# Performance work log

Measured on AMD Instinct MI355X. Metric: run time of the kernel, lower is better.

## Reference

```python
import jax, jax.numpy as jnp
import numpy as np

B, C, H, W = 16, 512, 32, 32
EPS = 1e-5

def setup_inputs() -> dict:
    key = jax.random.key(0)
    ks = jax.random.split(key, 7)
    s = 1.0 / np.sqrt(C)
    return {
        "x": jax.random.normal(ks[0], (B, C, H, W), dtype=jnp.float32),
        "norm_w": jnp.ones((C,), jnp.float32),
        "norm_b": jnp.zeros((C,), jnp.float32),
        "qkv_w": jax.random.normal(ks[1], (3 * C, C), dtype=jnp.float32) * s,
        "qkv_b": jax.random.normal(ks[2], (3 * C,), dtype=jnp.float32) * 0.01,
        "out_w": jax.random.normal(ks[3], (C, C), dtype=jnp.float32) * s,
        "out_b": jax.random.normal(ks[4], (C,), dtype=jnp.float32) * 0.01,
    }

def reference(x, norm_w, norm_b, qkv_w, qkv_b, out_w, out_b):
    b, c, h, w = x.shape
    # GroupNorm with num_groups=1: normalize over (C,H,W) per sample, per-channel affine
    mean = jnp.mean(x, axis=(1, 2, 3), keepdims=True)
    var = jnp.var(x, axis=(1, 2, 3), keepdims=True)
    xn = (x - mean) * jax.lax.rsqrt(var + EPS)
    xn = xn * norm_w[None, :, None, None] + norm_b[None, :, None, None]
    # 1x1 conv QKV: [b,3c,h,w]
    qkv = jnp.einsum('bchw,oc->bohw', xn, qkv_w) + qkv_b[None, :, None, None]
    q, k, v = jnp.split(qkv, 3, axis=1)
    n = h * w
    q = q.transpose(0, 2, 3, 1).reshape(b, n, c)   # [b, N, c]
    k = k.reshape(b, c, n)                          # [b, c, N]
    v = v.transpose(0, 2, 3, 1).reshape(b, n, c)   # [b, N, c]
    scores = jnp.einsum('bnc,bcm->bnm', q, k) * (c ** -0.5)  # [b, N, N]
    attn = jax.nn.softmax(scores, axis=-1)
    out = jnp.einsum('bnm,bmc->bnc', attn, v)       # [b, N, c]
    out = out.reshape(b, h, w, c).transpose(0, 3, 1, 2)
    out = jnp.einsum('bchw,oc->bohw', out, out_w) + out_b[None, :, None, None]
    return out + x
```

## Files before the change

### kernel.cpp

```cpp
#include <hip/hip_runtime.h>
#include <math.h>

#define BATCH 16
#define CH    512
#define NTOK  1024
#define CHW   (CH * NTOK)
#define EPSV  1e-5f

typedef __attribute__((ext_vector_type(8))) short bf16x8;
typedef __attribute__((ext_vector_type(4))) float f32x4;

__device__ __forceinline__ unsigned short f2bf(float f) {
    union { float f; unsigned u; } cv; cv.f = f;
    unsigned r = cv.u + 0x7FFFu + ((cv.u >> 16) & 1u);
    return (unsigned short)(r >> 16);
}

static const size_t OFF_WQKV = 256;
static const size_t OFF_OW   = OFF_WQKV + 1572864;
static const size_t OFF_XNT  = OFF_OW   + 524288;
static const size_t OFF_QT   = OFF_XNT  + 16777216;
static const size_t OFF_KT   = OFF_QT   + 16777216;
static const size_t OFF_V    = OFF_KT   + 16777216;
static const size_t OFF_OT   = OFF_V    + 16777216;
static const size_t OFF_S    = OFF_OT   + 16777216;
static const size_t OFF_P    = OFF_S    + 67108864;

__global__ void k_zero_stats(float* ws) {
    if (threadIdx.x < 64) ws[threadIdx.x] = 0.0f;
}

__global__ __launch_bounds__(256) void k_stats_partial(const float* __restrict__ x, float* __restrict__ ws) {
    int blk   = blockIdx.x;
    int b     = blk >> 6;
    int chunk = blk & 63;
    const float4* xp = (const float4*)(x + (size_t)b * CHW + (size_t)chunk * 8192);
    int t = threadIdx.x;
    float s = 0.0f, ss = 0.0f;
#pragma unroll
    for (int j = 0; j < 8; j++) {
        float4 v = xp[t + j * 256];
        s  += v.x + v.y + v.z + v.w;
        ss += v.x * v.x + v.y * v.y + v.z * v.z + v.w * v.w;
    }
#pragma unroll
    for (int off = 32; off; off >>= 1) {
        s  += __shfl_xor(s, off, 64);
        ss += __shfl_xor(ss, off, 64);
    }
    __shared__ float ls[4], lss[4];
    int wave = t >> 6, lane = t & 63;
    if (lane == 0) { ls[wave] = s; lss[wave] = ss; }
    __syncthreads();
    if (t == 0) {
        atomicAdd(&ws[b], ls[0] + ls[1] + ls[2] + ls[3]);
        atomicAdd(&ws[16 + b], lss[0] + lss[1] + lss[2] + lss[3]);
    }
}

__global__ void k_stats_final(float* ws) {
    int b = threadIdx.x;
    if (b < 16) {
        float inv  = 1.0f / (float)CHW;
        float mean = ws[b] * inv;
        float var  = ws[16 + b] * inv - mean * mean;
        ws[32 + b] = mean;
        ws[48 + b] = rsqrtf(var + EPSV);
    }
}

__global__ __launch_bounds__(256) void k_cvt(const float* __restrict__ in, unsigned short* __restrict__ out, int n4) {
    int i = blockIdx.x * 256 + threadIdx.x;
    if (i < n4) {
        float4 v = ((const float4*)in)[i];
        ushort4 o;
        o.x = f2bf(v.x); o.y = f2bf(v.y); o.z = f2bf(v.z); o.w = f2bf(v.w);
        ((ushort4*)out)[i] = o;
    }
}

__global__ __launch_bounds__(256) void k_xnt(const float* __restrict__ x,
                                             const float* __restrict__ nw,
                                             const float* __restrict__ nb,
                                             const float* __restrict__ ws,
                                             unsigned short* __restrict__ xnt) {
    __shared__ float ls[64][65];
    int b  = blockIdx.z;
    int c0 = blockIdx.y * 64;
    int n0 = blockIdx.x * 64;
    float mean = ws[32 + b], rstd = ws[48 + b];
    int t = threadIdx.x;
    int cl = t >> 4, n4 = t & 15;
    const float* xb = x + (size_t)b * CHW;
#pragma unroll
    for (int i = 0; i < 4; i++) {
        int c = c0 + cl + i * 16;
        float a  = rstd * nw[c];
        float bb = nb[c] - mean * a;
        float4 v = *(const float4*)(xb + (size_t)c * NTOK + n0 + n4 * 4);
        ls[cl + i * 16][n4 * 4 + 0] = v.x * a + bb;
        ls[cl + i * 16][n4 * 4 + 1] = v.y * a + bb;
        ls[cl + i * 16][n4 * 4 + 2] = v.z * a + bb;
        ls[cl + i * 16][n4 * 4 + 3] = v.w * a + bb;
    }
    __syncthreads();
    int nl = t >> 4, c4 = t & 15;
    unsigned short* dst = xnt + (size_t)b * NTOK * CH;
#pragma unroll
    for (int i = 0; i < 4; i++) {
        int n = n0 + nl + i * 16;
        ushort4 o;
        o.x = f2bf(ls[c4 * 4 + 0][nl + i * 16]);
        o.y = f2bf(ls[c4 * 4 + 1][nl + i * 16]);
        o.z = f2bf(ls[c4 * 4 + 2][nl + i * 16]);
        o.w = f2bf(ls[c4 * 4 + 3][nl + i * 16]);
        *(ushort4*)(dst + (size_t)n * CH + c0 + c4 * 4) = o;
    }
}

__device__ __forceinline__ void mfma_core(const unsigned short* __restrict__ A, int lda,
                                          const unsigned short* __restrict__ B, int ldb,
                                          int K, int m0, int n0,
                                          unsigned short* sA, unsigned short* sB,
                                          f32x4 acc[4][4]) {
    const int t = threadIdx.x;
    const int w = t >> 6, lane = t & 63;
    const int wm = (w & 1) * 64, wn = (w >> 1) * 64;
    const int r16 = lane & 15, quad = lane >> 4;
#pragma unroll
    for (int i = 0; i < 4; i++)
#pragma unroll
        for (int j = 0; j < 4; j++) acc[i][j] = (f32x4){0.f, 0.f, 0.f, 0.f};
    const int row0 = t >> 2, kc0 = (t & 3) * 8;
    for (int k0 = 0; k0 < K; k0 += 32) {
        *(uint4*)(sA + (row0)      * 32 + kc0) = *(const uint4*)(A + (size_t)(m0 + row0)      * lda + k0 + kc0);
        *(uint4*)(sA + (row0 + 64) * 32 + kc0) = *(const uint4*)(A + (size_t)(m0 + row0 + 64) * lda + k0 + kc0);
        *(uint4*)(sB + (row0)      * 32 + kc0) = *(const uint4*)(B + (size_t)(n0 + row0)      * ldb + k0 + kc0);
        *(uint4*)(sB + (row0 + 64) * 32 + kc0) = *(const uint4*)(B + (size_t)(n0 + row0 + 64) * ldb + k0 + kc0);
        __syncthreads();
        bf16x8 af[4], bfr[4];
#pragma unroll
        for (int i = 0; i < 4; i++) af[i]  = *(const bf16x8*)(sA + (wm + i * 16 + r16) * 32 + quad * 8);
#pragma unroll
        for (int j = 0; j < 4; j++) bfr[j] = *(const bf16x8*)(sB + (wn + j * 16 + r16) * 32 + quad * 8);
#pragma unroll
        for (int i = 0; i < 4; i++)
#pragma unroll
            for (int j = 0; j < 4; j++)
                acc[i][j] = __builtin_amdgcn_mfma_f32_16x16x32_bf16(af[i], bfr[j], acc[i][j], 0, 0, 0);
        __syncthreads();
    }
}

__global__ __launch_bounds__(256) void k_gemm_qkv(const unsigned short* __restrict__ Wq,
                                                  const float* __restrict__ qb,
                                                  const unsigned short* __restrict__ XNT,
                                                  unsigned short* __restrict__ QT,
                                                  unsigned short* __restrict__ KT,
                                                  unsigned short* __restrict__ V) {
    __shared__ __align__(16) unsigned short sA[128 * 32];
    __shared__ __align__(16) unsigned short sB[128 * 32];
    const int b  = blockIdx.z;
    const int m0 = blockIdx.y * 128;
    const int n0 = blockIdx.x * 128;
    f32x4 acc[4][4];
    mfma_core(Wq, CH, XNT + (size_t)b * NTOK * CH, CH, CH, m0, n0, sA, sB, acc);
    const int t = threadIdx.x;
    const int w = t >> 6, lane = t & 63;
    const int wm = (w & 1) * 64, wn = (w >> 1) * 64;
    const int r16 = lane & 15, quad = lane >> 4;
    const int region = m0 >> 9;
    unsigned short* dstT = (region == 0) ? QT : KT;
#pragma unroll
    for (int i = 0; i < 4; i++) {
        const int o0g = m0 + wm + i * 16 + quad * 4;
        const int ro  = o0g & 511;
#pragma unroll
        for (int j = 0; j < 4; j++) {
            const int col = n0 + wn + j * 16 + r16;
            f32x4 a = acc[i][j];
            if (region < 2) {
                ushort4 pk;
                pk.x = f2bf(a[0] + qb[o0g + 0]);
                pk.y = f2bf(a[1] + qb[o0g + 1]);
                pk.z = f2bf(a[2] + qb[o0g + 2]);
                pk.w = f2bf(a[3] + qb[o0g + 3]);
                *(ushort4*)(dstT + (size_t)b * NTOK * CH + (size_t)col * CH + ro) = pk;
            } else {
#pragma unroll
                for (int r = 0; r < 4; r++)
                    V[(size_t)b * CH * NTOK + (size_t)(ro + r) * NTOK + col] = f2bf(a[r] + qb[o0g + r]);
            }
        }
    }
}

__global__ __launch_bounds__(256) void k_gemm_sc(const unsigned short* __restrict__ QT,
                                                 const unsigned short* __restrict__ KT,
                                                 float* __restrict__ S) {
    __shared__ __align__(16) unsigned short sA[128 * 32];
    __shared__ __align__(16) unsigned short sB[128 * 32];
    const int b  = blockIdx.z;
    const int m0 = blockIdx.y * 128;
    const int n0 = blockIdx.x * 128;
    f32x4 acc[4][4];
    mfma_core(QT + (size_t)b * NTOK * CH, CH, KT + (size_t)b * NTOK * CH, CH, CH, m0, n0, sA, sB, acc);
    const int t = threadIdx.x;
    const int w = t >> 6, lane = t & 63;
    const int wm = (w & 1) * 64, wn = (w >> 1) * 64;
    const int r16 = lane & 15, quad = lane >> 4;
    const float scale = 0.044194173824159216f;
    float* Sb = S + (size_t)b * NTOK * NTOK;
#pragma unroll
    for (int i = 0; i < 4; i++) {
        const int row0 = m0 + wm + i * 16 + quad * 4;
#pragma unroll
        for (int j = 0; j < 4; j++) {
            const int col = n0 + wn + j * 16 + r16;
            f32x4 a = acc[i][j];
#pragma unroll
            for (int r = 0; r < 4; r++)
                Sb[(size_t)(row0 + r) * NTOK + col] = a[r] * scale;
        }
    }
}

__global__ __launch_bounds__(256) void k_softmax(const float* __restrict__ S, unsigned short* __restrict__ P) {
    size_t row = blockIdx.x;
    const float* p = S + row * NTOK;
    unsigned short* q = P + row * NTOK;
    int t = threadIdx.x;
    int wave = t >> 6, lane = t & 63;
    __shared__ float red[4];
    float4 v = ((const float4*)p)[t];
    float m = fmaxf(fmaxf(v.x, v.y), fmaxf(v.z, v.w));
#pragma unroll
    for (int off = 32; off; off >>= 1) m = fmaxf(m, __shfl_xor(m, off, 64));
    if (lane == 0) red[wave] = m;
    __syncthreads();
    m = fmaxf(fmaxf(red[0], red[1]), fmaxf(red[2], red[3]));
    __syncthreads();
    v.x = __expf(v.x - m);
    v.y = __expf(v.y - m);
    v.z = __expf(v.z - m);
    v.w = __expf(v.w - m);
    float s = v.x + v.y + v.z + v.w;
#pragma unroll
    for (int off = 32; off; off >>= 1) s += __shfl_xor(s, off, 64);
    if (lane == 0) red[wave] = s;
    __syncthreads();
    s = red[0] + red[1] + red[2] + red[3];
    float inv = 1.0f / s;
    ushort4 o;
    o.x = f2bf(v.x * inv); o.y = f2bf(v.y * inv); o.z = f2bf(v.z * inv); o.w = f2bf(v.w * inv);
    ((ushort4*)q)[t] = o;
}

__global__ __launch_bounds__(256) void k_gemm_av(const unsigned short* __restrict__ V,
                                                 const unsigned short* __restrict__ P,
                                                 unsigned short* __restrict__ OT) {
    __shared__ __align__(16) unsigned short sA[128 * 32];
    __shared__ __align__(16) unsigned short sB[128 * 32];
    const int b  = blockIdx.z;
    const int m0 = blockIdx.y * 128;
    const int n0 = blockIdx.x * 128;
    f32x4 acc[4][4];
    mfma_core(V + (size_t)b * CH * NTOK, NTOK, P + (size_t)b * NTOK * NTOK, NTOK, NTOK, m0, n0, sA, sB, acc);
    const int t = threadIdx.x;
    const int w = t >> 6, lane = t & 63;
    const int wm = (w & 1) * 64, wn = (w >> 1) * 64;
    const int r16 = lane & 15, quad = lane >> 4;
    unsigned short* OTb = OT + (size_t)b * NTOK * CH;
#pragma unroll
    for (int i = 0; i < 4; i++) {
        const int c0g = m0 + wm + i * 16 + quad * 4;
#pragma unroll
        for (int j = 0; j < 4; j++) {
            const int col = n0 + wn + j * 16 + r16;
            f32x4 a = acc[i][j];
            ushort4 pk;
            pk.x = f2bf(a[0]); pk.y = f2bf(a[1]); pk.z = f2bf(a[2]); pk.w = f2bf(a[3]);
            *(ushort4*)(OTb + (size_t)col * CH + c0g) = pk;
        }
    }
}

__global__ __launch_bounds__(256) void k_gemm_out(const unsigned short* __restrict__ OW,
                                                  const float* __restrict__ ob,
                                                  const unsigned short* __restrict__ OT,
                                                  const float* __restrict__ x,
                                                  float* __restrict__ out) {
    __shared__ __align__(16) unsigned short sA[128 * 32];
    __shared__ __align__(16) unsigned short sB[128 * 32];
    const int b  = blockIdx.z;
    const int m0 = blockIdx.y * 128;
    const int n0 = blockIdx.x * 128;
    f32x4 acc[4][4];
    mfma_core(OW, CH, OT + (size_t)b * NTOK * CH, CH, CH, m0, n0, sA, sB, acc);
    const int t = threadIdx.x;
    const int w = t >> 6, lane = t & 63;
    const int wm = (w & 1) * 64, wn = (w >> 1) * 64;
    const int r16 = lane & 15, quad = lane >> 4;
#pragma unroll
    for (int i = 0; i < 4; i++) {
        const int o0g = m0 + wm + i * 16 + quad * 4;
#pragma unroll
        for (int j = 0; j < 4; j++) {
            const int col = n0 + wn + j * 16 + r16;
            f32x4 a = acc[i][j];
#pragma unroll
            for (int r = 0; r < 4; r++) {
                size_t idx = (size_t)b * CHW + (size_t)(o0g + r) * NTOK + col;
                out[idx] = a[r] + ob[o0g + r] + x[idx];
            }
        }
    }
}

extern "C" void kernel_launch(void* const* d_in, const int* in_sizes, int n_in,
                              void* d_out, int out_size, void* d_ws, size_t ws_size,
                              hipStream_t stream) {
    const float* x      = (const float*)d_in[0];
    const float* norm_w = (const float*)d_in[1];
    const float* norm_b = (const float*)d_in[2];
    const float* qkv_w  = (const float*)d_in[3];
    const float* qkv_b  = (const float*)d_in[4];
    const float* out_w  = (const float*)d_in[5];
    const float* out_b  = (const float*)d_in[6];
    float* out = (float*)d_out;
    char* wsb  = (char*)d_ws;

    float* stats = (float*)wsb;
    unsigned short* WQ  = (unsigned short*)(wsb + OFF_WQKV);
    unsigned short* OW  = (unsigned short*)(wsb + OFF_OW);
    unsigned short* XNT = (unsigned short*)(wsb + OFF_XNT);
    unsigned short* QT  = (unsigned short*)(wsb + OFF_QT);
    unsigned short* KT  = (unsigned short*)(wsb + OFF_KT);
    unsigned short* V   = (unsigned short*)(wsb + OFF_V);
    unsigned short* OT  = (unsigned short*)(wsb + OFF_OT);
    float*          S   = (float*)(wsb + OFF_S);
    unsigned short* P   = (unsigned short*)(wsb + OFF_P);

    k_zero_stats<<<1, 64, 0, stream>>>(stats);
    k_stats_partial<<<BATCH * 64, 256, 0, stream>>>(x, stats);
    k_stats_final<<<1, 16, 0, stream>>>(stats);
    k_cvt<<<768, 256, 0, stream>>>(qkv_w, WQ, 3 * CH * CH / 4);
    k_cvt<<<256, 256, 0, stream>>>(out_w, OW, CH * CH / 4);
    k_xnt<<<dim3(NTOK / 64, CH / 64, BATCH), 256, 0, stream>>>(x, norm_w, norm_b, stats, XNT);
    k_gemm_qkv<<<dim3(NTOK / 128, 3 * CH / 128, BATCH), 256, 0, stream>>>(WQ, qkv_b, XNT, QT, KT, V);
    k_gemm_sc<<<dim3(NTOK / 128, NTOK / 128, BATCH), 256, 0, stream>>>(QT, KT, S);
    k_softmax<<<BATCH * NTOK, 256, 0, stream>>>(S, P);
    k_gemm_av<<<dim3(NTOK / 128, CH / 128, BATCH), 256, 0, stream>>>(V, P, OT);
    k_gemm_out<<<dim3(NTOK / 128, CH / 128, BATCH), 256, 0, stream>>>(OW, out_b, OT, x, out);
}
```

Measured before the change: 279.4 us.

## Load GEMM tiles directly into LDS and store attention scores as bf16

The shared GEMM core now uses global_load_lds async copies to move each 16-byte chunk straight from global memory into LDS, bypassing registers. Separately, the score matrix S is written as bf16 instead of fp32 and softmax reads bf16, halving the dominant intermediate traffic and shrinking its workspace. The bf16 scores lose precision before the softmax, and the async load layout depends on per-wave row mapping matching the LDS tile layout.

Result: faster. 266.2 us (-4.7%).

```diff
diff --git a/kernel.cpp b/kernel.cpp
--- a/kernel.cpp
+++ b/kernel.cpp
@@ -14,6 +14,17 @@
     union { float f; unsigned u; } cv; cv.f = f;
     unsigned r = cv.u + 0x7FFFu + ((cv.u >> 16) & 1u);
     return (unsigned short)(r >> 16);
+}
+__device__ __forceinline__ float bf2f(unsigned short u) {
+    union { unsigned u; float f; } cv; cv.u = ((unsigned)u) << 16;
+    return cv.f;
+}
+
+__device__ __forceinline__ void async16(const unsigned short* g, unsigned short* l) {
+    __builtin_amdgcn_global_load_lds(
+        (const __attribute__((address_space(1))) void*)g,
+        (__attribute__((address_space(3))) void*)l,
+        16, 0, 0);
 }
 
 static const size_t OFF_WQKV = 256;
@@ -24,7 +35,7 @@
 static const size_t OFF_V    = OFF_KT   + 16777216;
 static const size_t OFF_OT   = OFF_V    + 16777216;
 static const size_t OFF_S    = OFF_OT   + 16777216;
-static const size_t OFF_P    = OFF_S    + 67108864;
+static const size_t OFF_P    = OFF_S    + 33554432;
 
 __global__ void k_zero_stats(float* ws) {
     if (threadIdx.x < 64) ws[threadIdx.x] = 0.0f;
@@ -131,12 +142,21 @@
     for (int i = 0; i < 4; i++)
 #pragma unroll
         for (int j = 0; j < 4; j++) acc[i][j] = (f32x4){0.f, 0.f, 0.f, 0.f};
-    const int row0 = t >> 2, kc0 = (t & 3) * 8;
+    const int sr = lane >> 2;
+    const int sk = (lane & 3) * 8;
+    const unsigned short* gA0 = A + (size_t)(m0 + w * 32 + sr) * lda + sk;
+    const unsigned short* gA1 = gA0 + (size_t)16 * lda;
+    const unsigned short* gB0 = B + (size_t)(n0 + w * 32 + sr) * ldb + sk;
+    const unsigned short* gB1 = gB0 + (size_t)16 * ldb;
+    unsigned short* lA0 = sA + (w * 32)      * 32;
+    unsigned short* lA1 = sA + (w * 32 + 16) * 32;
+    unsigned short* lB0 = sB + (w * 32)      * 32;
+    unsigned short* lB1 = sB + (w * 32 + 16) * 32;
     for (int k0 = 0; k0 < K; k0 += 32) {
-        *(uint4*)(sA + (row0)      * 32 + kc0) = *(const uint4*)(A + (size_t)(m0 + row0)      * lda + k0 + kc0);
-        *(uint4*)(sA + (row0 + 64) * 32 + kc0) = *(const uint4*)(A + (size_t)(m0 + row0 + 64) * lda + k0 + kc0);
-        *(uint4*)(sB + (row0)      * 32 + kc0) = *(const uint4*)(B + (size_t)(n0 + row0)      * ldb + k0 + kc0);
-        *(uint4*)(sB + (row0 + 64) * 32 + kc0) = *(const uint4*)(B + (size_t)(n0 + row0 + 64) * ldb + k0 + kc0);
+        async16(gA0 + k0, lA0);
+        async16(gA1 + k0, lA1);
+        async16(gB0 + k0, lB0);
+        async16(gB1 + k0, lB1);
         __syncthreads();
         bf16x8 af[4], bfr[4];
 #pragma unroll
@@ -197,7 +217,7 @@
 
 __global__ __launch_bounds__(256) void k_gemm_sc(const unsigned short* __restrict__ QT,
                                                  const unsigned short* __restrict__ KT,
-                                                 float* __restrict__ S) {
+                                                 unsigned short* __restrict__ S) {
     __shared__ __align__(16) unsigned short sA[128 * 32];
     __shared__ __align__(16) unsigned short sB[128 * 32];
     const int b  = blockIdx.z;
@@ -210,7 +230,7 @@
     const int wm = (w & 1) * 64, wn = (w >> 1) * 64;
     const int r16 = lane & 15, quad = lane >> 4;
     const float scale = 0.044194173824159216f;
-    float* Sb = S + (size_t)b * NTOK * NTOK;
+    unsigned short* Sb = S + (size_t)b * NTOK * NTOK;
 #pragma unroll
     for (int i = 0; i < 4; i++) {
         const int row0 = m0 + wm + i * 16 + quad * 4;
@@ -220,19 +240,21 @@
             f32x4 a = acc[i][j];
 #pragma unroll
             for (int r = 0; r < 4; r++)
-                Sb[(size_t)(row0 + r) * NTOK + col] = a[r] * scale;
+                Sb[(size_t)(row0 + r) * NTOK + col] = f2bf(a[r] * scale);
         }
     }
 }
 
-__global__ __launch_bounds__(256) void k_softmax(const float* __restrict__ S, unsigned short* __restrict__ P) {
+__global__ __launch_bounds__(256) void k_softmax(const unsigned short* __restrict__ S, unsigned short* __restrict__ P) {
     size_t row = blockIdx.x;
-    const float* p = S + row * NTOK;
+    const unsigned short* p = S + row * NTOK;
     unsigned short* q = P + row * NTOK;
     int t = threadIdx.x;
     int wave = t >> 6, lane = t & 63;
     __shared__ float red[4];
-    float4 v = ((const float4*)p)[t];
+    ushort4 u = ((const ushort4*)p)[t];
+    float4 v;
+    v.x = bf2f(u.x); v.y = bf2f(u.y); v.z = bf2f(u.z); v.w = bf2f(u.w);
     float m = fmaxf(fmaxf(v.x, v.y), fmaxf(v.z, v.w));
 #pragma unroll
     for (int off = 32; off; off >>= 1) m = fmaxf(m, __shfl_xor(m, off, 64));
@@ -338,7 +360,7 @@
     unsigned short* KT  = (unsigned short*)(wsb + OFF_KT);
     unsigned short* V   = (unsigned short*)(wsb + OFF_V);
     unsigned short* OT  = (unsigned short*)(wsb + OFF_OT);
-    float*          S   = (float*)(wsb + OFF_S);
+    unsigned short* S   = (unsigned short*)(wsb + OFF_S);
     unsigned short* P   = (unsigned short*)(wsb + OFF_P);
 
     k_zero_stats<<<1, 64, 0, stream>>>(stats);
```
